# Kernel tuning notes

Measured on AMD Instinct MI355X. Metric: run time of the kernel, lower is better.

## Reference

```python
import jax, jax.numpy as jnp
import numpy as np

N_NODES = 100000
N_EDGES = 1600000
IN_CH = 3
HID = 32
BN_EPS = 1e-5


def setup_inputs() -> dict:
    key = jax.random.key(0)
    k_x, k_e1, k_e2, k_w, k_b, k_p = jax.random.split(key, 6)
    x = jax.random.normal(k_x, (N_NODES, IN_CH), dtype=jnp.float32)
    src = jax.random.randint(k_e1, (N_EDGES,), 0, N_NODES)
    dst = jax.random.randint(k_e2, (N_EDGES,), 0, N_NODES)
    edge_index = jnp.stack([src, dst]).astype(jnp.int64)
    # GCNConv linear params (glorot-ish init)
    W = jax.random.normal(k_w, (IN_CH, HID), dtype=jnp.float32) / np.sqrt(IN_CH)
    b = jnp.zeros((HID,), dtype=jnp.float32)
    bn_gamma = jnp.ones((HID,), dtype=jnp.float32)
    bn_beta = jnp.zeros((HID,), dtype=jnp.float32)
    prelu_w = jnp.full((1,), 0.25, dtype=jnp.float32)  # torch PReLU default
    return {"x": x, "edge_index": edge_index, "W": W, "b": b,
            "bn_gamma": bn_gamma, "bn_beta": bn_beta, "prelu_w": prelu_w}


def reference(x, edge_index, W, b, bn_gamma, bn_beta, prelu_w):
    src, dst = edge_index[0], edge_index[1]
    n = x.shape[0]
    # --- GCNConv: sym-normalized aggregation with self-loops ---
    # degree including self loop (edge weights = 1)
    deg = 1.0 + jax.ops.segment_sum(jnp.ones_like(src, dtype=x.dtype), dst,
                                    num_segments=n)
    dinv = jax.lax.rsqrt(deg)                       # deg^{-1/2}, [N]
    h = x @ W                                       # [N, HID]
    norm = dinv[src] * dinv[dst]                    # [E]
    msg = h[src] * norm[:, None]                    # [E, HID] gather
    agg = jax.ops.segment_sum(msg, dst, num_segments=n)  # scatter-add
    agg = agg + h * (1.0 / deg)[:, None]            # self-loop term
    agg = agg + b
    # --- BatchNorm1d (training-mode batch statistics, biased var) ---
    mean = jnp.mean(agg, axis=0)
    var = jnp.mean(jnp.square(agg - mean), axis=0)
    xhat = (agg - mean) * jax.lax.rsqrt(var + BN_EPS)
    y = xhat * bn_gamma + bn_beta
    # --- PReLU (single shared slope) ---
    y = jnp.where(y >= 0, y, prelu_w[0] * y)
    # dropout(p=0.5) is identity in eval / deterministic reference
    return y
```

## Files before the change

### kernel.cpp

```cpp
#include <hip/hip_runtime.h>

#define N_NODES 100000
#define N_EDGES 1600000
#define HID 32
#define BN_EPS 1e-5f

#define EPB   4096
#define NBLK  391
#define BSZ   512
#define NBUCK 196
#define SRC_MASK 0x1FFFFu


__global__ void bin_kernel(const int* __restrict__ src, const int* __restrict__ dst,
                           unsigned* __restrict__ staged, int* __restrict__ blen,
                           int* __restrict__ boffs) {
    __shared__ int hist[NBUCK], offs[NBUCK], curs[NBUCK];
    __shared__ int sc[256];
    __shared__ unsigned stage[EPB];
    int tid = threadIdx.x, blk = blockIdx.x;
    int e0 = blk * EPB;
    int cnt = N_EDGES - e0; if (cnt > EPB) cnt = EPB;

    unsigned pk[8]; int bk[8];
#pragma unroll
    for (int i = 0; i < 8; ++i) {
        int j = tid + i * 512;
        if (j < cnt) {
            int e = e0 + j;
            int d = dst[e];
            bk[i] = d >> 9;
            pk[i] = ((unsigned)(d & (BSZ - 1)) << 17) | (unsigned)src[e];
        } else bk[i] = -1;
    }
    for (int j = tid; j < NBUCK; j += 512) hist[j] = 0;
    __syncthreads();
#pragma unroll
    for (int i = 0; i < 8; ++i)
        if (bk[i] >= 0) atomicAdd(&hist[bk[i]], 1);
    __syncthreads();
    int h = (tid < NBUCK) ? hist[tid] : 0;
    if (tid < 256) sc[tid] = h;
    __syncthreads();
    for (int off = 1; off < 256; off <<= 1) {
        int v = 0;
        if (tid < 256 && tid >= off) v = sc[tid - off];
        __syncthreads();
        if (tid < 256) sc[tid] += v;
        __syncthreads();
    }
    if (tid < NBUCK) { int ex = sc[tid] - h; offs[tid] = ex; curs[tid] = ex; }
    __syncthreads();
#pragma unroll
    for (int i = 0; i < 8; ++i)
        if (bk[i] >= 0) {
            int p = atomicAdd(&curs[bk[i]], 1);
            stage[p] = pk[i];
        }
    __syncthreads();
    for (int j = tid; j < cnt; j += 512) staged[e0 + j] = stage[j];
    for (int j = tid; j < NBUCK; j += 512) {
        blen[j * NBLK + blk]  = hist[j];
        boffs[j * NBLK + blk] = e0 + offs[j];
    }
}

__global__ void scan1_kernel(const int* __restrict__ blen, int* __restrict__ runoff,
                             int* __restrict__ tot) {
    __shared__ int sc[512];
    int tid = threadIdx.x, b = blockIdx.x;
    int v = (tid < NBLK) ? blen[b * NBLK + tid] : 0;
    sc[tid] = v;
    __syncthreads();
    for (int off = 1; off < 512; off <<= 1) {
        int t = (tid >= off) ? sc[tid - off] : 0;
        __syncthreads();
        sc[tid] += t;
        __syncthreads();
    }
    if (tid < NBLK) runoff[b * NBLK + tid] = sc[tid] - v;
    if (tid == 511) tot[b] = sc[511];
}

__global__ void scan2_kernel(const int* __restrict__ tot, int* __restrict__ bstart) {
    __shared__ int sc[256];
    int tid = threadIdx.x;
    int v = (tid < NBUCK) ? tot[tid] : 0;
    sc[tid] = v;
    __syncthreads();
    for (int off = 1; off < 256; off <<= 1) {
        int t = (tid >= off) ? sc[tid - off] : 0;
        __syncthreads();
        sc[tid] += t;
        __syncthreads();
    }
    if (tid < NBUCK) bstart[tid] = sc[tid] - v;
    if (tid == 255) bstart[NBUCK] = sc[255];
}

__global__ void scatter2_kernel(const unsigned* __restrict__ staged, const int* __restrict__ blen,
                                const int* __restrict__ boffs, const int* __restrict__ runoff,
                                const int* __restrict__ bstart, const float* __restrict__ x,
                                unsigned* __restrict__ bbuf2, float4* __restrict__ xd) {
    __shared__ int hist[BSZ];
    __shared__ int l_len[NBLK], l_soff[NBLK], l_doff[NBLK];
    int tid = threadIdx.x, b = blockIdx.x;
    int bs = bstart[b];
    for (int j = tid; j < BSZ; j += 1024) hist[j] = 0;
    for (int j = tid; j < NBLK; j += 1024) {
        l_len[j]  = blen[b * NBLK + j];
        l_soff[j] = boffs[b * NBLK + j];
        l_doff[j] = bs + runoff[b * NBLK + j];
    }
    __syncthreads();
    int wv = tid >> 6, lane = tid & 63;
    for (int r = wv; r < NBLK; r += 16) {
        int len = l_len[r];
        int so = l_soff[r], dof = l_doff[r];
        for (int k = lane; k < len; k += 64) {
            unsigned p = staged[so + k];
            bbuf2[dof + k] = p;
            atomicAdd(&hist[p >> 17], 1);
        }
    }
    __syncthreads();
    if (tid < BSZ) {
        int n = (b << 9) + tid;
        if (n < N_NODES) {
            float rd = rsqrtf(1.0f + (float)hist[tid]);
            xd[n] = make_float4(x[3 * n] * rd, x[3 * n + 1] * rd, x[3 * n + 2] * rd, rd);
        }
    }
}

__global__ void accum_kernel(const unsigned* __restrict__ bbuf2, const int* __restrict__ bstart,
                             const float4* __restrict__ xd, float4* __restrict__ S4,
                             float* __restrict__ stats) {
    __shared__ float S[BSZ * 3];
    __shared__ float ls[16][9];
    int tid = threadIdx.x, b = blockIdx.x;
    for (int j = tid; j < BSZ * 3; j += 1024) S[j] = 0.f;
    __syncthreads();
    int e0 = bstart[b], e1 = bstart[b + 1];
    for (int e = e0 + tid; e < e1; e += 1024) {
        unsigned p = bbuf2[e];
        float4 v = xd[p & SRC_MASK];
        int l3 = (int)(p >> 17) * 3;
        atomicAdd(&S[l3 + 0], v.x);
        atomicAdd(&S[l3 + 1], v.y);
        atomicAdd(&S[l3 + 2], v.z);
    }
    __syncthreads();
    float st[9];
#pragma unroll
    for (int q = 0; q < 9; ++q) st[q] = 0.f;
    if (tid < BSZ) {
        int n = (b << 9) + tid;
        if (n < N_NODES) {
            float4 self = xd[n];
            float sx = S[tid * 3 + 0] + self.x;
            float sy = S[tid * 3 + 1] + self.y;
            float sz = S[tid * 3 + 2] + self.z;
            S4[n] = make_float4(sx, sy, sz, self.w);
            float ax = self.w * sx, ay = self.w * sy, az = self.w * sz;
            st[0] = ax; st[1] = ay; st[2] = az;
            st[3] = ax * ax; st[4] = ax * ay; st[5] = ax * az;
            st[6] = ay * ay; st[7] = ay * az; st[8] = az * az;
        }
    }
    for (int m = 1; m < 64; m <<= 1)
#pragma unroll
        for (int q = 0; q < 9; ++q) st[q] += __shfl_xor(st[q], m);
    int wv = tid >> 6;
    if ((tid & 63) == 0)
#pragma unroll
        for (int q = 0; q < 9; ++q) ls[wv][q] = st[q];
    __syncthreads();
    if (tid < 9) {
        float s = 0.f;
#pragma unroll
        for (int w = 0; w < 16; ++w) s += ls[w][tid];
        atomicAdd(&stats[tid], s);
    }
}

__global__ void final_out_kernel(const float4* __restrict__ S4, const float* __restrict__ stats,
                                 const float* __restrict__ W, const float* __restrict__ bb,
                                 const float* __restrict__ gamma, const float* __restrict__ beta,
                                 const float* __restrict__ prelu, float* __restrict__ out) {
    __shared__ float cb[4 * HID];
    int tid = threadIdx.x;
    if (tid < HID) {
        int c = tid;
        float m1x = stats[0], m1y = stats[1], m1z = stats[2];
        float Mxx = stats[3], Mxy = stats[4], Mxz = stats[5];
        float Myy = stats[6], Myz = stats[7], Mzz = stats[8];
        float w0 = W[c], w1 = W[HID + c], w2 = W[2 * HID + c];
        const float invn = 1.0f / (float)N_NODES;
        float m1w = m1x * w0 + m1y * w1 + m1z * w2;
        float mean = m1w * invn + bb[c];
        float quad = w0 * w0 * Mxx + w1 * w1 * Myy + w2 * w2 * Mzz
                   + 2.f * (w0 * w1 * Mxy + w0 * w2 * Mxz + w1 * w2 * Myz);
        float ex2 = quad * invn + 2.f * bb[c] * m1w * invn + bb[c] * bb[c];
        float var = ex2 - mean * mean;
        float sc = gamma[c] * rsqrtf(var + BN_EPS);
        cb[c] = w0 * sc;
        cb[HID + c] = w1 * sc;
        cb[2 * HID + c] = w2 * sc;
        cb[3 * HID + c] = bb[c] * sc + (beta[c] - mean * sc);
    }
    __syncthreads();
    float a = prelu[0];
    int stride = gridDim.x * blockDim.x;
    for (int t = blockIdx.x * blockDim.x + tid; t < N_NODES * HID; t += stride) {
        int n = t >> 5, c = t & 31;
        float4 s = S4[n];
        float y = s.w * (s.x * cb[c] + s.y * cb[HID + c] + s.z * cb[2 * HID + c])
                + cb[3 * HID + c];
        out[t] = y >= 0.f ? y : a * y;
    }
}


__global__ void fb_count_kernel(const int* __restrict__ dst, int* __restrict__ cnt) {
    int e = blockIdx.x * blockDim.x + threadIdx.x;
    if (e < N_EDGES) atomicAdd(&cnt[dst[e]], 1);
}

__global__ void fb_xd_kernel(const float* __restrict__ x, const int* __restrict__ cnt,
                             float4* __restrict__ xd, float4* __restrict__ S4) {
    int n = blockIdx.x * blockDim.x + threadIdx.x;
    if (n >= N_NODES) return;
    float rd = rsqrtf(1.0f + (float)cnt[n]);
    float4 v = make_float4(x[3 * n] * rd, x[3 * n + 1] * rd, x[3 * n + 2] * rd, rd);
    xd[n] = v;
    S4[n] = v;
}

__global__ void fb_scatter_kernel(const int* __restrict__ src, const int* __restrict__ dst,
                                  const float4* __restrict__ xd, float4* __restrict__ S4) {
    int e = blockIdx.x * blockDim.x + threadIdx.x;
    if (e >= N_EDGES) return;
    int s = src[e], d = dst[e];
    float4 v = xd[s];
    float* p = (float*)&S4[d];
    atomicAdd(p + 0, v.x);
    atomicAdd(p + 1, v.y);
    atomicAdd(p + 2, v.z);
}

__global__ void fb_stats_kernel(const float4* __restrict__ S4, float* __restrict__ stats) {
    __shared__ float ls[4][9];
    int tid = threadIdx.x;
    int n = blockIdx.x * blockDim.x + tid;
    float st[9];
#pragma unroll
    for (int q = 0; q < 9; ++q) st[q] = 0.f;
    if (n < N_NODES) {
        float4 s = S4[n];
        float ax = s.w * s.x, ay = s.w * s.y, az = s.w * s.z;
        st[0] = ax; st[1] = ay; st[2] = az;
        st[3] = ax * ax; st[4] = ax * ay; st[5] = ax * az;
        st[6] = ay * ay; st[7] = ay * az; st[8] = az * az;
    }
    for (int m = 1; m < 64; m <<= 1)
#pragma unroll
        for (int q = 0; q < 9; ++q) st[q] += __shfl_xor(st[q], m);
    int wv = tid >> 6;
    if ((tid & 63) == 0)
#pragma unroll
        for (int q = 0; q < 9; ++q) ls[wv][q] = st[q];
    __syncthreads();
    if (tid < 9) {
        float s = ls[0][tid] + ls[1][tid] + ls[2][tid] + ls[3][tid];
        atomicAdd(&stats[tid], s);
    }
}


extern "C" void kernel_launch(void* const* d_in, const int* in_sizes, int n_in,
                              void* d_out, int out_size, void* d_ws, size_t ws_size,
                              hipStream_t stream) {
    const float* x     = (const float*)d_in[0];
    const int*   ei    = (const int*)d_in[1];
    const float* W     = (const float*)d_in[2];
    const float* b     = (const float*)d_in[3];
    const float* gamma = (const float*)d_in[4];
    const float* beta  = (const float*)d_in[5];
    const float* prelu = (const float*)d_in[6];

    const int* src = ei;
    const int* dst = ei + N_EDGES;
    char* ws = (char*)d_ws;
    float* out = (float*)d_out;

    const size_t NEEDED = 16927456;

    if (ws_size >= NEEDED) {
        float*    stats  = (float*)(ws);
        int*      tot    = (int*)(ws + 64);
        int*      bstart = (int*)(ws + 848);
        int*      blen   = (int*)(ws + 1664);
        int*      boffs  = (int*)(ws + 308208);
        int*      runoff = (int*)(ws + 614752);
        unsigned* staged = (unsigned*)(ws + 921312);
        unsigned* bbuf2  = (unsigned*)(ws + 7327456);
        float4*   xd     = (float4*)(ws + 13727456);
        float4*   S4     = (float4*)(ws + 15327456);

        hipMemsetAsync(stats, 0, 64, stream);
        bin_kernel<<<NBLK, 512, 0, stream>>>(src, dst, staged, blen, boffs);
        scan1_kernel<<<NBUCK, 512, 0, stream>>>(blen, runoff, tot);
        scan2_kernel<<<1, 256, 0, stream>>>(tot, bstart);
        scatter2_kernel<<<NBUCK, 1024, 0, stream>>>(staged, blen, boffs, runoff, bstart,
                                                    x, bbuf2, xd);
        accum_kernel<<<NBUCK, 1024, 0, stream>>>(bbuf2, bstart, xd, S4, stats);
        final_out_kernel<<<2048, 256, 0, stream>>>(S4, stats, W, b, gamma, beta, prelu, out);
    } else {
        int*    cnt   = (int*)(ws);
        float*  stats = (float*)(ws + 400000);
        float4* xd    = (float4*)(ws + 400640);
        float4* S4    = (float4*)(ws + 2000640);

        hipMemsetAsync(ws, 0, 400064, stream);
        fb_count_kernel<<<(N_EDGES + 255) / 256, 256, 0, stream>>>(dst, cnt);
        fb_xd_kernel<<<(N_NODES + 255) / 256, 256, 0, stream>>>(x, cnt, xd, S4);
        fb_scatter_kernel<<<(N_EDGES + 255) / 256, 256, 0, stream>>>(src, dst, xd, S4);
        fb_stats_kernel<<<(N_NODES + 255) / 256, 256, 0, stream>>>(S4, stats);
        final_out_kernel<<<2048, 256, 0, stream>>>(S4, stats, W, b, gamma, beta, prelu, out);
    }
}
```

Before: 147.5 us.

## Replace staged two-pass bucket sort with count-then-place binning into smaller buckets

The edge binning pipeline changes from a per-block local sort plus a staged copy into a count pass and a direct atomic placement pass over 256 edge slices. Bucket size drops from 512 to 256 nodes, so there are 391 buckets, and the degree computation moves into its own kernel that rereads the binned buffer. This removes the staged intermediate buffer and the memset, which the stats zeroing in scan2 replaces. In exchange, dst is read twice, the placement writes are scattered, and edge order within a bucket is no longer deterministic.

New measurement: 142.0 us. 3.7% less time.

```diff
diff --git a/kernel.cpp b/kernel.cpp
--- a/kernel.cpp
+++ b/kernel.cpp
@@ -5,127 +5,91 @@
 #define HID 32
 #define BN_EPS 1e-5f
 
-#define EPB   4096
-#define NBLK  391
-#define BSZ   512
-#define NBUCK 196
+#define BSZ    256
+#define NBUCK  391
+#define NSLICE 256
+#define EPS    6250
 #define SRC_MASK 0x1FFFFu
 
 
-__global__ void bin_kernel(const int* __restrict__ src, const int* __restrict__ dst,
-                           unsigned* __restrict__ staged, int* __restrict__ blen,
-                           int* __restrict__ boffs) {
-    __shared__ int hist[NBUCK], offs[NBUCK], curs[NBUCK];
-    __shared__ int sc[256];
-    __shared__ unsigned stage[EPB];
-    int tid = threadIdx.x, blk = blockIdx.x;
-    int e0 = blk * EPB;
-    int cnt = N_EDGES - e0; if (cnt > EPB) cnt = EPB;
-
-    unsigned pk[8]; int bk[8];
-#pragma unroll
-    for (int i = 0; i < 8; ++i) {
-        int j = tid + i * 512;
-        if (j < cnt) {
-            int e = e0 + j;
-            int d = dst[e];
-            bk[i] = d >> 9;
-            pk[i] = ((unsigned)(d & (BSZ - 1)) << 17) | (unsigned)src[e];
-        } else bk[i] = -1;
-    }
-    for (int j = tid; j < NBUCK; j += 512) hist[j] = 0;
-    __syncthreads();
-#pragma unroll
-    for (int i = 0; i < 8; ++i)
-        if (bk[i] >= 0) atomicAdd(&hist[bk[i]], 1);
-    __syncthreads();
-    int h = (tid < NBUCK) ? hist[tid] : 0;
-    if (tid < 256) sc[tid] = h;
-    __syncthreads();
-    for (int off = 1; off < 256; off <<= 1) {
-        int v = 0;
-        if (tid < 256 && tid >= off) v = sc[tid - off];
-        __syncthreads();
-        if (tid < 256) sc[tid] += v;
-        __syncthreads();
-    }
-    if (tid < NBUCK) { int ex = sc[tid] - h; offs[tid] = ex; curs[tid] = ex; }
-    __syncthreads();
-#pragma unroll
-    for (int i = 0; i < 8; ++i)
-        if (bk[i] >= 0) {
-            int p = atomicAdd(&curs[bk[i]], 1);
-            stage[p] = pk[i];
-        }
-    __syncthreads();
-    for (int j = tid; j < cnt; j += 512) staged[e0 + j] = stage[j];
-    for (int j = tid; j < NBUCK; j += 512) {
-        blen[j * NBLK + blk]  = hist[j];
-        boffs[j * NBLK + blk] = e0 + offs[j];
-    }
-}
-
-__global__ void scan1_kernel(const int* __restrict__ blen, int* __restrict__ runoff,
+__global__ void count_kernel(const int* __restrict__ dst, int* __restrict__ cnt) {
+    __shared__ int hist[NBUCK];
+    int tid = threadIdx.x, s = blockIdx.x;
+    for (int j = tid; j < NBUCK; j += 1024) hist[j] = 0;
+    __syncthreads();
+    int e0 = s * EPS, e1 = e0 + EPS;
+    if (e1 > N_EDGES) e1 = N_EDGES;
+    for (int e = e0 + tid; e < e1; e += 1024)
+        atomicAdd(&hist[dst[e] >> 8], 1);
+    __syncthreads();
+    for (int j = tid; j < NBUCK; j += 1024) cnt[s * NBUCK + j] = hist[j];
+}
+
+__global__ void scan1_kernel(const int* __restrict__ cnt, int* __restrict__ runoff,
                              int* __restrict__ tot) {
+    __shared__ int sc[NSLICE];
+    int t = threadIdx.x, b = blockIdx.x;
+    int v = cnt[t * NBUCK + b];
+    sc[t] = v;
+    __syncthreads();
+    for (int off = 1; off < NSLICE; off <<= 1) {
+        int u = (t >= off) ? sc[t - off] : 0;
+        __syncthreads();
+        sc[t] += u;
+        __syncthreads();
+    }
+    runoff[t * NBUCK + b] = sc[t] - v;
+    if (t == NSLICE - 1) tot[b] = sc[t];
+}
+
+__global__ void scan2_kernel(const int* __restrict__ tot, int* __restrict__ bstart,
+                             float* __restrict__ stats) {
     __shared__ int sc[512];
+    int t = threadIdx.x;
+    int v = (t < NBUCK) ? tot[t] : 0;
+    sc[t] = v;
+    __syncthreads();
+    for (int off = 1; off < 512; off <<= 1) {
+        int u = (t >= off) ? sc[t - off] : 0;
+        __syncthreads();
+        sc[t] += u;
+        __syncthreads();
+    }
+    if (t < NBUCK) bstart[t] = sc[t] - v;
+    if (t == 0) bstart[NBUCK] = N_EDGES;
+    if (t < 16) stats[t] = 0.f;
+}
+
+__global__ void place_kernel(const int* __restrict__ src, const int* __restrict__ dst,
+                             const int* __restrict__ runoff, const int* __restrict__ bstart,
+                             unsigned* __restrict__ bbuf2) {
+    __shared__ int curs[NBUCK];
+    int tid = threadIdx.x, s = blockIdx.x;
+    for (int j = tid; j < NBUCK; j += 1024)
+        curs[j] = bstart[j] + runoff[s * NBUCK + j];
+    __syncthreads();
+    int e0 = s * EPS, e1 = e0 + EPS;
+    if (e1 > N_EDGES) e1 = N_EDGES;
+    for (int e = e0 + tid; e < e1; e += 1024) {
+        int d = dst[e];
+        int b = d >> 8;
+        int p = atomicAdd(&curs[b], 1);
+        bbuf2[p] = ((unsigned)(d & 255) << 17) | (unsigned)src[e];
+    }
+}
+
+__global__ void degxd_kernel(const unsigned* __restrict__ bbuf2, const int* __restrict__ bstart,
+                             const float* __restrict__ x, float4* __restrict__ xd) {
+    __shared__ int hist[BSZ];
     int tid = threadIdx.x, b = blockIdx.x;
-    int v = (tid < NBLK) ? blen[b * NBLK + tid] : 0;
-    sc[tid] = v;
-    __syncthreads();
-    for (int off = 1; off < 512; off <<= 1) {
-        int t = (tid >= off) ? sc[tid - off] : 0;
-        __syncthreads();
-        sc[tid] += t;
-        __syncthreads();
-    }
-    if (tid < NBLK) runoff[b * NBLK + tid] = sc[tid] - v;
-    if (tid == 511) tot[b] = sc[511];
-}
-
-__global__ void scan2_kernel(const int* __restrict__ tot, int* __restrict__ bstart) {
-    __shared__ int sc[256];
-    int tid = threadIdx.x;
-    int v = (tid < NBUCK) ? tot[tid] : 0;
-    sc[tid] = v;
-    __syncthreads();
-    for (int off = 1; off < 256; off <<= 1) {
-        int t = (tid >= off) ? sc[tid - off] : 0;
-        __syncthreads();
-        sc[tid] += t;
-        __syncthreads();
-    }
-    if (tid < NBUCK) bstart[tid] = sc[tid] - v;
-    if (tid == 255) bstart[NBUCK] = sc[255];
-}
-
-__global__ void scatter2_kernel(const unsigned* __restrict__ staged, const int* __restrict__ blen,
-                                const int* __restrict__ boffs, const int* __restrict__ runoff,
-                                const int* __restrict__ bstart, const float* __restrict__ x,
-                                unsigned* __restrict__ bbuf2, float4* __restrict__ xd) {
-    __shared__ int hist[BSZ];
-    __shared__ int l_len[NBLK], l_soff[NBLK], l_doff[NBLK];
-    int tid = threadIdx.x, b = blockIdx.x;
-    int bs = bstart[b];
-    for (int j = tid; j < BSZ; j += 1024) hist[j] = 0;
-    for (int j = tid; j < NBLK; j += 1024) {
-        l_len[j]  = blen[b * NBLK + j];
-        l_soff[j] = boffs[b * NBLK + j];
-        l_doff[j] = bs + runoff[b * NBLK + j];
-    }
-    __syncthreads();
-    int wv = tid >> 6, lane = tid & 63;
-    for (int r = wv; r < NBLK; r += 16) {
-        int len = l_len[r];
-        int so = l_soff[r], dof = l_doff[r];
-        for (int k = lane; k < len; k += 64) {
-            unsigned p = staged[so + k];
-            bbuf2[dof + k] = p;
-            atomicAdd(&hist[p >> 17], 1);
-        }
-    }
+    for (int j = tid; j < BSZ; j += 512) hist[j] = 0;
+    __syncthreads();
+    int e0 = bstart[b], e1 = bstart[b + 1];
+    for (int e = e0 + tid; e < e1; e += 512)
+        atomicAdd(&hist[bbuf2[e] >> 17], 1);
     __syncthreads();
     if (tid < BSZ) {
-        int n = (b << 9) + tid;
+        int n = (b << 8) + tid;
         if (n < N_NODES) {
             float rd = rsqrtf(1.0f + (float)hist[tid]);
             xd[n] = make_float4(x[3 * n] * rd, x[3 * n + 1] * rd, x[3 * n + 2] * rd, rd);
@@ -137,12 +101,12 @@
                              const float4* __restrict__ xd, float4* __restrict__ S4,
                              float* __restrict__ stats) {
     __shared__ float S[BSZ * 3];
-    __shared__ float ls[16][9];
+    __shared__ float ls[8][9];
     int tid = threadIdx.x, b = blockIdx.x;
-    for (int j = tid; j < BSZ * 3; j += 1024) S[j] = 0.f;
+    for (int j = tid; j < BSZ * 3; j += 512) S[j] = 0.f;
     __syncthreads();
     int e0 = bstart[b], e1 = bstart[b + 1];
-    for (int e = e0 + tid; e < e1; e += 1024) {
+    for (int e = e0 + tid; e < e1; e += 512) {
         unsigned p = bbuf2[e];
         float4 v = xd[p & SRC_MASK];
         int l3 = (int)(p >> 17) * 3;
@@ -155,7 +119,7 @@
 #pragma unroll
     for (int q = 0; q < 9; ++q) st[q] = 0.f;
     if (tid < BSZ) {
-        int n = (b << 9) + tid;
+        int n = (b << 8) + tid;
         if (n < N_NODES) {
             float4 self = xd[n];
             float sx = S[tid * 3 + 0] + self.x;
@@ -179,7 +143,7 @@
     if (tid < 9) {
         float s = 0.f;
 #pragma unroll
-        for (int w = 0; w < 16; ++w) s += ls[w][tid];
+        for (int w = 0; w < 8; ++w) s += ls[w][tid];
         atomicAdd(&stats[tid], s);
     }
 }
@@ -294,27 +258,24 @@
     char* ws = (char*)d_ws;
     float* out = (float*)d_out;
 
-    const size_t NEEDED = 16927456;
+    const size_t NEEDED = 10403968;
 
     if (ws_size >= NEEDED) {
         float*    stats  = (float*)(ws);
         int*      tot    = (int*)(ws + 64);
-        int*      bstart = (int*)(ws + 848);
-        int*      blen   = (int*)(ws + 1664);
-        int*      boffs  = (int*)(ws + 308208);
-        int*      runoff = (int*)(ws + 614752);
-        unsigned* staged = (unsigned*)(ws + 921312);
-        unsigned* bbuf2  = (unsigned*)(ws + 7327456);
-        float4*   xd     = (float4*)(ws + 13727456);
-        float4*   S4     = (float4*)(ws + 15327456);
-
-        hipMemsetAsync(stats, 0, 64, stream);
-        bin_kernel<<<NBLK, 512, 0, stream>>>(src, dst, staged, blen, boffs);
-        scan1_kernel<<<NBUCK, 512, 0, stream>>>(blen, runoff, tot);
-        scan2_kernel<<<1, 256, 0, stream>>>(tot, bstart);
-        scatter2_kernel<<<NBUCK, 1024, 0, stream>>>(staged, blen, boffs, runoff, bstart,
-                                                    x, bbuf2, xd);
-        accum_kernel<<<NBUCK, 1024, 0, stream>>>(bbuf2, bstart, xd, S4, stats);
+        int*      bstart = (int*)(ws + 1632);
+        int*      cnt    = (int*)(ws + 3200);
+        int*      runoff = (int*)(ws + 403584);
+        unsigned* bbuf2  = (unsigned*)(ws + 803968);
+        float4*   xd     = (float4*)(ws + 7203968);
+        float4*   S4     = (float4*)(ws + 8803968);
+
+        count_kernel<<<NSLICE, 1024, 0, stream>>>(dst, cnt);
+        scan1_kernel<<<NBUCK, NSLICE, 0, stream>>>(cnt, runoff, tot);
+        scan2_kernel<<<1, 512, 0, stream>>>(tot, bstart, stats);
+        place_kernel<<<NSLICE, 1024, 0, stream>>>(src, dst, runoff, bstart, bbuf2);
+        degxd_kernel<<<NBUCK, 512, 0, stream>>>(bbuf2, bstart, x, xd);
+        accum_kernel<<<NBUCK, 512, 0, stream>>>(bbuf2, bstart, xd, S4, stats);
         final_out_kernel<<<2048, 256, 0, stream>>>(S4, stats, W, b, gamma, beta, prelu, out);
     } else {
         int*    cnt   = (int*)(ws);
```
